# Kernel optimization log

Hardware: AMD Instinct MI355X
Metric: run time of the kernel (lower is better)

Reference implementation:

```python
import jax, jax.numpy as jnp
import numpy as np

B, N, CIN, COUT = 2, 4096, 128, 64

def setup_inputs() -> dict:
    key = jax.random.key(0)
    ks = jax.random.split(key, 9)
    s1 = 1.0 / np.sqrt(CIN)
    s2 = 1.0 / np.sqrt(COUT)
    sa = 1.0 / np.sqrt(2 * COUT)
    return {
        "x": jax.random.normal(ks[0], (B, N, CIN), dtype=jnp.float32),
        "adj_matrix": jax.random.uniform(ks[1], (B, N, N), dtype=jnp.float32),
        "W1": jax.random.uniform(ks[2], (CIN, COUT), jnp.float32, -s1, s1),
        "b1": jax.random.uniform(ks[3], (COUT,), jnp.float32, -s1, s1),
        "W2": jax.random.uniform(ks[4], (COUT, COUT), jnp.float32, -s2, s2),
        "b2": jax.random.uniform(ks[5], (COUT,), jnp.float32, -s2, s2),
        "Wa": jax.random.uniform(ks[6], (2 * COUT, 1), jnp.float32, -sa, sa),
        "ba": jax.random.uniform(ks[7], (1,), jnp.float32, -sa, sa),
    }

def reference(x, adj_matrix, W1, b1, W2, b2, Wa, ba):
    # conv: two Linear+ReLU layers -> h [B,N,C]
    h = jax.nn.relu(jnp.einsum('bni,io->bno', x, W1) + b1)
    h = jax.nn.relu(jnp.einsum('bni,io->bno', h, W2) + b2)
    # attention Linear(2C,1) on cat[h_i, h_j] factorizes: e_ij = sigmoid(u_i + v_j + b)
    C = h.shape[-1]
    u = jnp.einsum('bnc,c->bn', h, Wa[:C, 0])  # contribution of node i (row)
    v = jnp.einsum('bnc,c->bn', h, Wa[C:, 0])  # contribution of node j (col)
    e = jax.nn.sigmoid(u[:, :, None] + v[:, None, :] + ba[0])  # [B,N,N]
    a = e * adj_matrix
    a = a / (jnp.sum(a, axis=-1, keepdims=True) + 1e-10)
    h_out = jnp.einsum('bnm,bmc->bnc', a, h)
    return (h_out, a)
```

## Files before the change

kernel.cpp:

```cpp
#include <hip/hip_runtime.h>

#define BB 2
#define NN 4096
#define CIN 128
#define CC 64

typedef __attribute__((ext_vector_type(4))) float floatx4;
typedef __attribute__((ext_vector_type(8))) short short8;

__device__ __forceinline__ short f2bf(float f) {
    unsigned u = __float_as_uint(f);
    u += 0x7fffu + ((u >> 16) & 1u);
    return (short)(u >> 16);
}

__device__ __forceinline__ float sigf(float x) {
    return __builtin_amdgcn_rcpf(1.0f + __expf(-x));
}

__global__ __launch_bounds__(256) void feat_v2(
    const float* __restrict__ x, const float* __restrict__ W1,
    const float* __restrict__ b1, const float* __restrict__ W2,
    const float* __restrict__ b2, const float* __restrict__ Wa,
    const float* __restrict__ ba,
    short* __restrict__ hT, float* __restrict__ u, float* __restrict__ v)
{
    __shared__ float W1s[CIN * CC];
    __shared__ float W2s[CC * CC];
    __shared__ float xs[16 * 132];
    __shared__ float h1s[16 * 68];

    const int t = threadIdx.x;
    const int row0 = blockIdx.x * 16;

    {
        const floatx4* s1 = (const floatx4*)W1;
        floatx4* d1 = (floatx4*)W1s;
        for (int i = t; i < CIN * CC / 4; i += 256) d1[i] = s1[i];
        const floatx4* s2 = (const floatx4*)W2;
        floatx4* d2 = (floatx4*)W2s;
        for (int i = t; i < CC * CC / 4; i += 256) d2[i] = s2[i];
        const floatx4* sx = (const floatx4*)(x + (size_t)row0 * CIN);
        for (int i = t; i < 16 * CIN / 4; i += 256) {
            int rw = i >> 5, c4 = i & 31;
            *(floatx4*)(xs + rw * 132 + c4 * 4) = sx[i];
        }
    }
    __syncthreads();

    const int n  = t >> 4;
    const int cg = t & 15;
    const int c0 = cg * 4;

    float acc[4];
#pragma unroll
    for (int i = 0; i < 4; i++) acc[i] = b1[c0 + i];
    for (int k = 0; k < CIN; k++) {
        float a = xs[n * 132 + k];
        const floatx4 w = *(const floatx4*)&W1s[k * CC + c0];
#pragma unroll
        for (int i = 0; i < 4; i++) acc[i] = fmaf(a, w[i], acc[i]);
    }
#pragma unroll
    for (int i = 0; i < 4; i++) h1s[n * 68 + c0 + i] = fmaxf(acc[i], 0.0f);
    __syncthreads();

    float acc2[4];
#pragma unroll
    for (int i = 0; i < 4; i++) acc2[i] = b2[c0 + i];
    for (int k = 0; k < CC; k++) {
        float a = h1s[n * 68 + k];
        const floatx4 w = *(const floatx4*)&W2s[k * CC + c0];
#pragma unroll
        for (int i = 0; i < 4; i++) acc2[i] = fmaf(a, w[i], acc2[i]);
    }
#pragma unroll
    for (int i = 0; i < 4; i++) acc2[i] = fmaxf(acc2[i], 0.0f);

    float pu = 0.0f, pv = 0.0f;
#pragma unroll
    for (int i = 0; i < 4; i++) {
        pu = fmaf(acc2[i], Wa[c0 + i], pu);
        pv = fmaf(acc2[i], Wa[CC + c0 + i], pv);
    }
    pu += __shfl_down(pu, 8, 16); pv += __shfl_down(pv, 8, 16);
    pu += __shfl_down(pu, 4, 16); pv += __shfl_down(pv, 4, 16);
    pu += __shfl_down(pu, 2, 16); pv += __shfl_down(pv, 2, 16);
    pu += __shfl_down(pu, 1, 16); pv += __shfl_down(pv, 1, 16);

    const int grow = row0 + n;
    if (cg == 0) { u[grow] = pu + ba[0]; v[grow] = pv; }

    const int b  = grow >> 12;
    const int nn = grow & (NN - 1);
#pragma unroll
    for (int i = 0; i < 4; i++)
        hT[((size_t)(b * CC + c0 + i)) * NN + nn] = f2bf(acc2[i]);
}

__global__ __launch_bounds__(256) void rowsum_v2(
    const float* __restrict__ adj, const float* __restrict__ u,
    const float* __restrict__ v, float* __restrict__ r)
{
    const int wave = threadIdx.x >> 6;
    const int lane = threadIdx.x & 63;
    const int row  = blockIdx.x * 4 + wave;
    const int b = row >> 12;
    const float un = u[row];
    const floatx4* arow = (const floatx4*)(adj + (size_t)row * NN);
    const floatx4* vb = (const floatx4*)(v + b * NN);

    float p0 = 0.f, p1 = 0.f, p2 = 0.f, p3 = 0.f;
#pragma unroll 4
    for (int i = 0; i < 16; i++) {
        int idx = lane + i * 64;
        floatx4 a4 = arow[idx];
        floatx4 v4 = vb[idx];
        p0 = fmaf(a4.x, sigf(un + v4.x), p0);
        p1 = fmaf(a4.y, sigf(un + v4.y), p1);
        p2 = fmaf(a4.z, sigf(un + v4.z), p2);
        p3 = fmaf(a4.w, sigf(un + v4.w), p3);
    }
    float p = (p0 + p1) + (p2 + p3);
#pragma unroll
    for (int off = 32; off > 0; off >>= 1) p += __shfl_down(p, off);
    if (lane == 0) r[row] = p;
}

__global__ __launch_bounds__(256, 8) void attn_v2(
    const float* __restrict__ adj, const float* __restrict__ u,
    const float* __restrict__ v, const float* __restrict__ r,
    const short* __restrict__ hT,
    float* __restrict__ hout, float* __restrict__ aout)
{
    __shared__ float red[4][16][CC + 1];

    const int wave = threadIdx.x >> 6;
    const int lane = threadIdx.x & 63;
    const int quad = lane >> 4;
    const int m16  = lane & 15;

    const int tile = blockIdx.x >> 2;
    const int jq   = blockIdx.x & 3;
    const int row0 = tile * 16;
    const int b  = row0 >> 12;
    const int n0 = row0 & (NN - 1);
    const int n  = n0 + m16;

    const size_t rowbase = ((size_t)(b * NN + n)) * NN;
    const float un    = u[b * NN + n];
    const float inv_r = 1.0f / (r[b * NN + n] + 1e-10f);
    const float* vb = v + b * NN;

    floatx4 acc[4];
#pragma unroll
    for (int g = 0; g < 4; g++) acc[g] = (floatx4){0.f, 0.f, 0.f, 0.f};

    const int jbase = jq * 1024 + wave * 256;
#pragma unroll 2
    for (int step = 0; step < 8; step++) {
        const int jb = jbase + step * 32 + quad * 8;
        const float* ap = adj + rowbase + jb;
        floatx4 a0 = *(const floatx4*)ap;
        floatx4 a1 = *(const floatx4*)(ap + 4);
        floatx4 v0 = *(const floatx4*)(vb + jb);
        floatx4 v1 = *(const floatx4*)(vb + jb + 4);

        float av[8] = {a0.x, a0.y, a0.z, a0.w, a1.x, a1.y, a1.z, a1.w};
        float vv[8] = {v0.x, v0.y, v0.z, v0.w, v1.x, v1.y, v1.z, v1.w};

        floatx4 o0, o1;
        short8 af;
#pragma unroll
        for (int i = 0; i < 8; i++) {
            float s = av[i] * sigf(un + vv[i]) * inv_r;
            if (i < 4) o0[i] = s; else o1[i - 4] = s;
            af[i] = f2bf(s);
        }
        *(floatx4*)(aout + rowbase + jb)     = o0;
        *(floatx4*)(aout + rowbase + jb + 4) = o1;

#pragma unroll
        for (int g = 0; g < 4; g++) {
            const short8* bp = (const short8*)(hT + ((size_t)(b * CC + g * 16 + m16)) * NN + jb);
            acc[g] = __builtin_amdgcn_mfma_f32_16x16x32_bf16(af, *bp, acc[g], 0, 0, 0);
        }
    }

#pragma unroll
    for (int g = 0; g < 4; g++) {
        const int c = g * 16 + m16;
#pragma unroll
        for (int i = 0; i < 4; i++)
            red[wave][quad * 4 + i][c] = acc[g][i];
    }
    __syncthreads();

#pragma unroll
    for (int e = 0; e < 4; e++) {
        const int idx = threadIdx.x * 4 + e;
        const int rr = idx >> 6;
        const int c  = idx & 63;
        float s = red[0][rr][c] + red[1][rr][c] + red[2][rr][c] + red[3][rr][c];
        atomicAdd(&hout[((size_t)(b * NN + n0 + rr)) * CC + c], s);
    }
}

extern "C" void kernel_launch(void* const* d_in, const int* in_sizes, int n_in,
                              void* d_out, int out_size, void* d_ws, size_t ws_size,
                              hipStream_t stream) {
    (void)in_sizes; (void)n_in; (void)out_size; (void)ws_size;
    const float* x   = (const float*)d_in[0];
    const float* adj = (const float*)d_in[1];
    const float* W1  = (const float*)d_in[2];
    const float* b1  = (const float*)d_in[3];
    const float* W2  = (const float*)d_in[4];
    const float* b2  = (const float*)d_in[5];
    const float* Wa  = (const float*)d_in[6];
    const float* ba  = (const float*)d_in[7];

    float* hout = (float*)d_out;
    float* aout = hout + (size_t)BB * NN * CC;

    char* ws = (char*)d_ws;
    short* hT = (short*)ws;
    float* u  = (float*)(ws + (size_t)BB * CC * NN * sizeof(short));
    float* vv = u + BB * NN;
    float* r  = vv + BB * NN;

    hipMemsetAsync(d_out, 0, (size_t)BB * NN * CC * sizeof(float), stream);
    feat_v2<<<BB * NN / 16, 256, 0, stream>>>(x, W1, b1, W2, b2, Wa, ba, hT, u, vv);
    rowsum_v2<<<BB * NN / 4, 256, 0, stream>>>(adj, u, vv, r);
    attn_v2<<<(BB * NN / 16) * 4, 256, 0, stream>>>(adj, u, vv, r, hT, hout, aout);
}
```

Measured before the change: 313.4 us.

## Fuse row-sum into attention kernel, one block per 16-row tile, drop atomics

Removes the separate rowsum kernel. The attention kernel now computes the row normalizer itself: each block covers 16 full rows and makes a first pass over adj before the MFMA pass. Because each block owns its whole row range, hout is written directly, which removes the memset and the atomics. The kernel also adds software double-buffered loads, nontemporal stores for the a output, and a coalesced transposed hT store through LDS in the feature kernel. The second pass over adj should mostly hit cache, but the grid shrinks to 512 blocks with launch_bounds(256,2), which risks lower occupancy and less latency hiding.

```diff
diff --git a/kernel.cpp b/kernel.cpp
--- a/kernel.cpp
+++ b/kernel.cpp
@@ -18,7 +18,7 @@
     return __builtin_amdgcn_rcpf(1.0f + __expf(-x));
 }
 
-__global__ __launch_bounds__(256) void feat_v2(
+__global__ __launch_bounds__(256) void feat_v3(
     const float* __restrict__ x, const float* __restrict__ W1,
     const float* __restrict__ b1, const float* __restrict__ W2,
     const float* __restrict__ b2, const float* __restrict__ Wa,
@@ -29,6 +29,7 @@
     __shared__ float W2s[CC * CC];
     __shared__ float xs[16 * 132];
     __shared__ float h1s[16 * 68];
+    __shared__ __align__(16) short hs[CC][16];
 
     const int t = threadIdx.x;
     const int row0 = blockIdx.x * 16;
@@ -77,6 +78,9 @@
 #pragma unroll
     for (int i = 0; i < 4; i++) acc2[i] = fmaxf(acc2[i], 0.0f);
 
+#pragma unroll
+    for (int i = 0; i < 4; i++) hs[c0 + i][n] = f2bf(acc2[i]);
+
     float pu = 0.0f, pv = 0.0f;
 #pragma unroll
     for (int i = 0; i < 4; i++) {
@@ -91,101 +95,136 @@
     const int grow = row0 + n;
     if (cg == 0) { u[grow] = pu + ba[0]; v[grow] = pv; }
 
-    const int b  = grow >> 12;
-    const int nn = grow & (NN - 1);
-#pragma unroll
-    for (int i = 0; i < 4; i++)
-        hT[((size_t)(b * CC + c0 + i)) * NN + nn] = f2bf(acc2[i]);
-}
-
-__global__ __launch_bounds__(256) void rowsum_v2(
+    __syncthreads();
+    if (t < 128) {
+        const int c  = t >> 1;
+        const int hf = t & 1;
+        const int b   = row0 >> 12;
+        const int nn0 = row0 & (NN - 1);
+        *(short8*)(hT + ((size_t)(b * CC + c)) * NN + nn0 + hf * 8) =
+            *(const short8*)&hs[c][hf * 8];
+    }
+}
+
+__global__ __launch_bounds__(256, 2) void attn_v3(
     const float* __restrict__ adj, const float* __restrict__ u,
-    const float* __restrict__ v, float* __restrict__ r)
-{
-    const int wave = threadIdx.x >> 6;
-    const int lane = threadIdx.x & 63;
-    const int row  = blockIdx.x * 4 + wave;
-    const int b = row >> 12;
-    const float un = u[row];
-    const floatx4* arow = (const floatx4*)(adj + (size_t)row * NN);
-    const floatx4* vb = (const floatx4*)(v + b * NN);
-
-    float p0 = 0.f, p1 = 0.f, p2 = 0.f, p3 = 0.f;
-#pragma unroll 4
-    for (int i = 0; i < 16; i++) {
-        int idx = lane + i * 64;
-        floatx4 a4 = arow[idx];
-        floatx4 v4 = vb[idx];
-        p0 = fmaf(a4.x, sigf(un + v4.x), p0);
-        p1 = fmaf(a4.y, sigf(un + v4.y), p1);
-        p2 = fmaf(a4.z, sigf(un + v4.z), p2);
-        p3 = fmaf(a4.w, sigf(un + v4.w), p3);
-    }
-    float p = (p0 + p1) + (p2 + p3);
-#pragma unroll
-    for (int off = 32; off > 0; off >>= 1) p += __shfl_down(p, off);
-    if (lane == 0) r[row] = p;
-}
-
-__global__ __launch_bounds__(256, 8) void attn_v2(
-    const float* __restrict__ adj, const float* __restrict__ u,
-    const float* __restrict__ v, const float* __restrict__ r,
-    const short* __restrict__ hT,
+    const float* __restrict__ v, const short* __restrict__ hT,
     float* __restrict__ hout, float* __restrict__ aout)
 {
     __shared__ float red[4][16][CC + 1];
+    __shared__ float rsum[4][16];
+    __shared__ float rinv[16];
 
     const int wave = threadIdx.x >> 6;
     const int lane = threadIdx.x & 63;
+    const int row0 = blockIdx.x * 16;
+    const int b  = row0 >> 12;
+    const int n0 = row0 & (NN - 1);
+    const float* vb = v + b * NN;
+    const int jw = wave * 1024;
+
+    float psum[16];
+    {
+        floatx4 vA = *(const floatx4*)(vb + jw +       lane * 4);
+        floatx4 vB = *(const floatx4*)(vb + jw + 256 + lane * 4);
+        floatx4 vC = *(const floatx4*)(vb + jw + 512 + lane * 4);
+        floatx4 vD = *(const floatx4*)(vb + jw + 768 + lane * 4);
+#pragma unroll 4
+        for (int r = 0; r < 16; ++r) {
+            const float* ar = adj + ((size_t)(b * NN + n0 + r)) * NN + jw;
+            floatx4 aA = *(const floatx4*)(ar +       lane * 4);
+            floatx4 aB = *(const floatx4*)(ar + 256 + lane * 4);
+            floatx4 aC = *(const floatx4*)(ar + 512 + lane * 4);
+            floatx4 aD = *(const floatx4*)(ar + 768 + lane * 4);
+            const float ur = u[b * NN + n0 + r];
+            float p = 0.f;
+#pragma unroll
+            for (int i = 0; i < 4; ++i) {
+                p = fmaf(aA[i], sigf(ur + vA[i]), p);
+                p = fmaf(aB[i], sigf(ur + vB[i]), p);
+                p = fmaf(aC[i], sigf(ur + vC[i]), p);
+                p = fmaf(aD[i], sigf(ur + vD[i]), p);
+            }
+            psum[r] = p;
+        }
+    }
+#pragma unroll
+    for (int off = 32; off; off >>= 1) {
+#pragma unroll
+        for (int r = 0; r < 16; ++r) psum[r] += __shfl_down(psum[r], off);
+    }
+    if (lane == 0) {
+#pragma unroll
+        for (int r = 0; r < 16; ++r) rsum[wave][r] = psum[r];
+    }
+    __syncthreads();
+    if (threadIdx.x < 16) {
+        const int r = threadIdx.x;
+        float s = rsum[0][r] + rsum[1][r] + rsum[2][r] + rsum[3][r];
+        rinv[r] = __builtin_amdgcn_rcpf(s + 1e-10f);
+    }
+    __syncthreads();
+
     const int quad = lane >> 4;
     const int m16  = lane & 15;
-
-    const int tile = blockIdx.x >> 2;
-    const int jq   = blockIdx.x & 3;
-    const int row0 = tile * 16;
-    const int b  = row0 >> 12;
-    const int n0 = row0 & (NN - 1);
-    const int n  = n0 + m16;
-
+    const int n    = n0 + m16;
     const size_t rowbase = ((size_t)(b * NN + n)) * NN;
     const float un    = u[b * NN + n];
-    const float inv_r = 1.0f / (r[b * NN + n] + 1e-10f);
-    const float* vb = v + b * NN;
+    const float inv_r = rinv[m16];
+
+    const float* ap_base = adj + rowbase;
+    float*       op_base = aout + rowbase;
+    const short* hp0 = hT + ((size_t)(b * CC +  0 + m16)) * NN;
+    const short* hp1 = hT + ((size_t)(b * CC + 16 + m16)) * NN;
+    const short* hp2 = hT + ((size_t)(b * CC + 32 + m16)) * NN;
+    const short* hp3 = hT + ((size_t)(b * CC + 48 + m16)) * NN;
 
     floatx4 acc[4];
 #pragma unroll
     for (int g = 0; g < 4; g++) acc[g] = (floatx4){0.f, 0.f, 0.f, 0.f};
 
-    const int jbase = jq * 1024 + wave * 256;
-#pragma unroll 2
-    for (int step = 0; step < 8; step++) {
-        const int jb = jbase + step * 32 + quad * 8;
-        const float* ap = adj + rowbase + jb;
-        floatx4 a0 = *(const floatx4*)ap;
-        floatx4 a1 = *(const floatx4*)(ap + 4);
-        floatx4 v0 = *(const floatx4*)(vb + jb);
-        floatx4 v1 = *(const floatx4*)(vb + jb + 4);
-
-        float av[8] = {a0.x, a0.y, a0.z, a0.w, a1.x, a1.y, a1.z, a1.w};
-        float vv[8] = {v0.x, v0.y, v0.z, v0.w, v1.x, v1.y, v1.z, v1.w};
-
-        floatx4 o0, o1;
-        short8 af;
-#pragma unroll
-        for (int i = 0; i < 8; i++) {
-            float s = av[i] * sigf(un + vv[i]) * inv_r;
-            if (i < 4) o0[i] = s; else o1[i - 4] = s;
-            af[i] = f2bf(s);
-        }
-        *(floatx4*)(aout + rowbase + jb)     = o0;
-        *(floatx4*)(aout + rowbase + jb + 4) = o1;
-
-#pragma unroll
-        for (int g = 0; g < 4; g++) {
-            const short8* bp = (const short8*)(hT + ((size_t)(b * CC + g * 16 + m16)) * NN + jb);
-            acc[g] = __builtin_amdgcn_mfma_f32_16x16x32_bf16(af, *bp, acc[g], 0, 0, 0);
-        }
-    }
+    const int jb0 = jw + quad * 8;
+
+    floatx4 a0A, a1A, v0A, v1A; short8 h0A, h1A, h2A, h3A;
+    floatx4 a0B, a1B, v0B, v1B; short8 h0B, h1B, h2B, h3B;
+
+#define LOADST(S, jb) { \
+    a0##S = *(const floatx4*)(ap_base + (jb));      \
+    a1##S = *(const floatx4*)(ap_base + (jb) + 4);  \
+    v0##S = *(const floatx4*)(vb + (jb));           \
+    v1##S = *(const floatx4*)(vb + (jb) + 4);       \
+    h0##S = *(const short8*)(hp0 + (jb));           \
+    h1##S = *(const short8*)(hp1 + (jb));           \
+    h2##S = *(const short8*)(hp2 + (jb));           \
+    h3##S = *(const short8*)(hp3 + (jb)); }
+
+#define COMPST(S, jb) { \
+    float av[8] = {a0##S.x, a0##S.y, a0##S.z, a0##S.w, a1##S.x, a1##S.y, a1##S.z, a1##S.w}; \
+    float vv[8] = {v0##S.x, v0##S.y, v0##S.z, v0##S.w, v1##S.x, v1##S.y, v1##S.z, v1##S.w}; \
+    floatx4 o0, o1; short8 af; \
+    _Pragma("unroll") \
+    for (int i = 0; i < 8; ++i) { \
+        float s_ = av[i] * sigf(un + vv[i]) * inv_r; \
+        if (i < 4) o0[i] = s_; else o1[i - 4] = s_; \
+        af[i] = f2bf(s_); } \
+    __builtin_nontemporal_store(o0, (floatx4*)(op_base + (jb)));     \
+    __builtin_nontemporal_store(o1, (floatx4*)(op_base + (jb) + 4)); \
+    acc[0] = __builtin_amdgcn_mfma_f32_16x16x32_bf16(af, h0##S, acc[0], 0, 0, 0); \
+    acc[1] = __builtin_amdgcn_mfma_f32_16x16x32_bf16(af, h1##S, acc[1], 0, 0, 0); \
+    acc[2] = __builtin_amdgcn_mfma_f32_16x16x32_bf16(af, h2##S, acc[2], 0, 0, 0); \
+    acc[3] = __builtin_amdgcn_mfma_f32_16x16x32_bf16(af, h3##S, acc[3], 0, 0, 0); }
+
+    LOADST(A, jb0)
+    LOADST(B, jb0 + 32)
+#pragma unroll
+    for (int s = 0; s < 32; s += 2) {
+        COMPST(A, jb0 + s * 32)
+        if (s + 2 < 32) LOADST(A, jb0 + (s + 2) * 32)
+        COMPST(B, jb0 + (s + 1) * 32)
+        if (s + 3 < 32) LOADST(B, jb0 + (s + 3) * 32)
+    }
+#undef LOADST
+#undef COMPST
 
 #pragma unroll
     for (int g = 0; g < 4; g++) {
@@ -202,7 +241,7 @@
         const int rr = idx >> 6;
         const int c  = idx & 63;
         float s = red[0][rr][c] + red[1][rr][c] + red[2][rr][c] + red[3][rr][c];
-        atomicAdd(&hout[((size_t)(b * NN + n0 + rr)) * CC + c], s);
+        hout[((size_t)(b * NN + n0 + rr)) * CC + c] = s;
     }
 }
 
@@ -226,10 +265,7 @@
     short* hT = (short*)ws;
     float* u  = (float*)(ws + (size_t)BB * CC * NN * sizeof(short));
     float* vv = u + BB * NN;
-    float* r  = vv + BB * NN;
-
-    hipMemsetAsync(d_out, 0, (size_t)BB * NN * CC * sizeof(float), stream);
-    feat_v2<<<BB * NN / 16, 256, 0, stream>>>(x, W1, b1, W2, b2, Wa, ba, hT, u, vv);
-    rowsum_v2<<<BB * NN / 4, 256, 0, stream>>>(adj, u, vv, r);
-    attn_v2<<<(BB * NN / 16) * 4, 256, 0, stream>>>(adj, u, vv, r, hT, hout, aout);
-}
+
+    feat_v3<<<BB * NN / 16, 256, 0, stream>>>(x, W1, b1, W2, b2, Wa, ba, hT, u, vv);
+    attn_v3<<<BB * NN / 16, 256, 0, stream>>>(adj, u, vv, hT, hout, aout);
+}
```

After: 300.0 us. -4.3%, faster.
